# Performance work log

Measured on AMD Instinct MI355X. Metric: run time of the kernel, lower is better.

## Reference

```python
import jax, jax.numpy as jnp
import numpy as np

# Static module config (must match init_kwargs / input_specs)
C, HEADS, POINTS, LEVELS = 256, 8, 8, 2
H, W = 128, 128           # BEV grid per agent/level
NQ = H * W                # num_query = H*W
DH = C // HEADS           # per-head dim


def setup_inputs() -> dict:
    key = jax.random.key(0)
    ks = jax.random.split(key, 12)
    s = 0.02
    return {
        "query": jax.random.normal(ks[0], (1, NQ, C), jnp.float32),
        "query_pos": jax.random.normal(ks[1], (1, NQ, C), jnp.float32),
        "value": jax.random.normal(ks[2], (LEVELS, NQ, C), jnp.float32),
        "reference_points": jax.random.uniform(ks[3], (1, NQ, LEVELS, 2), jnp.float32),
        "spatial_shapes": jnp.full((LEVELS, 2), H, dtype=jnp.int32),
        "W_off": jax.random.normal(ks[4], (C, LEVELS * HEADS * POINTS * 2), jnp.float32) * s,
        "b_off": jax.random.normal(ks[5], (LEVELS * HEADS * POINTS * 2,), jnp.float32) * s,
        "W_attn": jax.random.normal(ks[6], (C, LEVELS * HEADS * POINTS), jnp.float32) * s,
        "b_attn": jax.random.normal(ks[7], (LEVELS * HEADS * POINTS,), jnp.float32) * s,
        "W_val": jax.random.normal(ks[8], (C, C), jnp.float32) * s,
        "b_val": jax.random.normal(ks[9], (C,), jnp.float32) * s,
        "W_out": jax.random.normal(ks[10], (C, C), jnp.float32) * s,
        "b_out": jax.random.normal(ks[11], (C,), jnp.float32) * s,
    }


def _bilinear(img, x, y):
    """grid_sample-style bilinear, align_corners=False, zero padding.
    img: (H, W, D); x, y: (...) pixel-space coords. Returns (..., D)."""
    Hh, Ww = img.shape[0], img.shape[1]
    x0f, y0f = jnp.floor(x), jnp.floor(y)
    x0, y0 = x0f.astype(jnp.int32), y0f.astype(jnp.int32)
    x1, y1 = x0 + 1, y0 + 1
    wx1, wy1 = x - x0f, y - y0f
    wx0, wy0 = 1.0 - wx1, 1.0 - wy1

    def gather(yy, xx):
        valid = (yy >= 0) & (yy < Hh) & (xx >= 0) & (xx < Ww)
        g = img[jnp.clip(yy, 0, Hh - 1), jnp.clip(xx, 0, Ww - 1)]
        return jnp.where(valid[..., None], g, 0.0)

    return (gather(y0, x0) * (wy0 * wx0)[..., None]
            + gather(y0, x1) * (wy0 * wx1)[..., None]
            + gather(y1, x0) * (wy1 * wx0)[..., None]
            + gather(y1, x1) * (wy1 * wx1)[..., None])


_sample_heads = jax.vmap(_bilinear, in_axes=(0, 0, 0))  # over heads


def reference(query, query_pos, value, reference_points, spatial_shapes,
              W_off, b_off, W_attn, b_attn, W_val, b_val, W_out, b_out):
    identity = query                                        # (1, NQ, C)
    q = (query + query_pos)[0]                              # (NQ, C), bs=1

    v = value @ W_val + b_val                               # (L, NQ, C)
    v = v.reshape(LEVELS, H, W, HEADS, DH)                  # per-level feature maps

    off = (q @ W_off + b_off).reshape(NQ, HEADS, LEVELS, POINTS, 2)
    attn = (q @ W_attn + b_attn).reshape(NQ, HEADS, LEVELS * POINTS)
    attn = jax.nn.softmax(attn, axis=-1).reshape(NQ, HEADS, LEVELS, POINTS)

    # offset_normalizer = (W, H) per level
    norm = jnp.stack([spatial_shapes[:, 1], spatial_shapes[:, 0]], -1).astype(q.dtype)  # (L, 2)
    # sampling_locations in normalized [0,1] coords: (NQ, HEADS, LEVELS, POINTS, 2)
    loc = reference_points[0][:, None, :, None, :] + off / norm[None, None, :, None, :]

    out = jnp.zeros((NQ, HEADS, DH), dtype=q.dtype)
    for l in range(LEVELS):
        img_l = jnp.transpose(v[l], (2, 0, 1, 3))           # (HEADS, H, W, DH)
        # align_corners=False: px = x_norm * W - 0.5
        xl = jnp.transpose(loc[:, :, l, :, 0], (1, 0, 2)) * W - 0.5  # (HEADS, NQ, POINTS)
        yl = jnp.transpose(loc[:, :, l, :, 1], (1, 0, 2)) * H - 0.5
        sampled = _sample_heads(img_l, xl, yl)              # (HEADS, NQ, POINTS, DH)
        out = out + jnp.einsum('hqpd,qhp->qhd', sampled, attn[:, :, l, :])

    out = out.reshape(NQ, C) @ W_out + b_out                # (NQ, C)
    return out[None] + identity                             # dropout is identity (eval / p=0)
```

## Files before the change

kernel.cpp:

```cpp
#include <hip/hip_runtime.h>
#include <hip/hip_bf16.h>
#include <math.h>

#define NQ     16384
#define CDIM   256
#define NHEADS 8
#define NPTS   8
#define NLVL   2
#define HH     128
#define WWID   128
#define DHEAD  32
#define NCAT   384

#define PW        130
#define CELLB     32
#define ROWB      (PW * CELLB)
#define MAPB      (PW * PW * CELLB)
#define BORDER_BLKS 16
#define TRANS_BLKS  224

typedef __bf16 bf16_t;
typedef __bf16 bf16x8 __attribute__((ext_vector_type(8)));
typedef float  f32x4  __attribute__((ext_vector_type(4)));
typedef float  f32x2  __attribute__((ext_vector_type(2)));

typedef __attribute__((address_space(1))) const uint32_t gau32;
typedef __attribute__((address_space(3))) uint32_t lau32;

__device__ __forceinline__ bf16_t f2b(float f) { return (bf16_t)f; }

__device__ __forceinline__ bf16x8 cvt8(float4 a, float4 b) {
    bf16x8 v;
    v[0] = f2b(a.x); v[1] = f2b(a.y); v[2] = f2b(a.z); v[3] = f2b(a.w);
    v[4] = f2b(b.x); v[5] = f2b(b.y); v[6] = f2b(b.z); v[7] = f2b(b.w);
    return v;
}

__global__ __launch_bounds__(256) void prep_k(const float* __restrict__ W_val,
                                              const float* __restrict__ W_off,
                                              const float* __restrict__ W_attn,
                                              const float* __restrict__ W_out,
                                              unsigned char* __restrict__ v2,
                                              bf16_t* __restrict__ Wt_val,
                                              bf16_t* __restrict__ Wt_qa,
                                              bf16_t* __restrict__ Wt_out) {
    const int b = blockIdx.x;
    if (b < BORDER_BLKS) {
        unsigned char* map = v2 + (size_t)b * MAPB;
        for (int i = threadIdx.x; i < 516; i += 256) {
            int y, x;
            if (i < 130)      { y = 0;        x = i;       }
            else if (i < 260) { y = 129;      x = i - 130; }
            else if (i < 388) { y = i - 259;  x = 0;       }
            else              { y = i - 387;  x = 129;     }
            uint4* p = reinterpret_cast<uint4*>(map + (size_t)y * ROWB + x * CELLB);
            p[0] = make_uint4(0, 0, 0, 0);
            p[1] = make_uint4(0, 0, 0, 0);
        }
        return;
    }
    {
        const int tb = b - BORDER_BLKS;
        const float* W; bf16_t* Wt; int N, t; bool permute = false;
        if (tb < 64)       { W = W_val;  Wt = Wt_val;            N = 256; t = tb;       permute = true; }
        else if (tb < 128) { W = W_off;  Wt = Wt_qa;             N = 256; t = tb - 64;  }
        else if (tb < 160) { W = W_attn; Wt = Wt_qa + 256 * 256; N = 128; t = tb - 128; }
        else               { W = W_out;  Wt = Wt_out;            N = 256; t = tb - 160; }
        const int ntn = N >> 5;
        const int k0 = (t / ntn) * 32, n0 = (t % ntn) * 32;
        const int tx = threadIdx.x & 31, ty = threadIdx.x >> 5;
        __shared__ float s[32][33];
#pragma unroll
        for (int i = 0; i < 4; ++i)
            s[ty + 8 * i][tx] = W[(size_t)(k0 + ty + 8 * i) * N + n0 + tx];
        __syncthreads();
#pragma unroll
        for (int i = 0; i < 4; ++i) {
            const int n = n0 + ty + 8 * i;
            const int p = permute ? ((n & ~63) | ((n & 3) << 4) | ((n & 63) >> 2)) : n;
            Wt[(size_t)p * 256 + k0 + tx] = f2b(s[tx][ty + 8 * i]);
        }
    }
}

template <int AMODE, bool PERM_V>
__device__ __forceinline__ void proj_body(bf16_t (&As)[2][64][64],
                                          int bidx, int bidy,
                                          const float* __restrict__ Af0,
                                          const float* __restrict__ Af1,
                                          const bf16_t* __restrict__ Bt,
                                          const float* __restrict__ bias,
                                          const float* __restrict__ bias2,
                                          int Nsplit,
                                          void* __restrict__ Cout,
                                          int N, int K) {
    const int tid  = threadIdx.x;
    const int wave = tid >> 6;
    const int lane = tid & 63;
    const int rowBase = bidy * 64;
    const int colBase = bidx * 128;
    const int wn = wave * 32;
    const int fr = lane & 15;
    const int fq = lane >> 4;

    f32x4 acc[4][2] = {};

    const int lrow = lane >> 3;
    const int scol = ((lane & 7) ^ lrow) * 8;

    auto loadA = [&](int t, float4 (&ra)[2][2]) {
#pragma unroll
        for (int tt = 0; tt < 2; ++tt) {
            const float* src =
                Af0 + (size_t)(rowBase + wave * 16 + tt * 8 + lrow) * K + t * 64 + scol;
            ra[tt][0] = *reinterpret_cast<const float4*>(src);
            ra[tt][1] = *reinterpret_cast<const float4*>(src + 4);
        }
    };
    auto loadA2 = [&](int t, float4 (&rb)[2][2]) {
#pragma unroll
        for (int tt = 0; tt < 2; ++tt) {
            const float* src =
                Af1 + (size_t)(rowBase + wave * 16 + tt * 8 + lrow) * K + t * 64 + scol;
            rb[tt][0] = *reinterpret_cast<const float4*>(src);
            rb[tt][1] = *reinterpret_cast<const float4*>(src + 4);
        }
    };
    auto storeA = [&](int buf, float4 (&ra)[2][2]) {
#pragma unroll
        for (int tt = 0; tt < 2; ++tt)
            *reinterpret_cast<bf16x8*>(
                &As[buf][wave * 16 + tt * 8 + lrow][(lane & 7) * 8]) =
                cvt8(ra[tt][0], ra[tt][1]);
    };
    auto storeAsum = [&](int buf, float4 (&ra)[2][2], float4 (&rb)[2][2]) {
#pragma unroll
        for (int tt = 0; tt < 2; ++tt) {
            float4 a = ra[tt][0], c = ra[tt][1];
            a.x += rb[tt][0].x; a.y += rb[tt][0].y;
            a.z += rb[tt][0].z; a.w += rb[tt][0].w;
            c.x += rb[tt][1].x; c.y += rb[tt][1].y;
            c.z += rb[tt][1].z; c.w += rb[tt][1].w;
            *reinterpret_cast<bf16x8*>(
                &As[buf][wave * 16 + tt * 8 + lrow][(lane & 7) * 8]) = cvt8(a, c);
        }
    };
    auto compute = [&](int c, int t) {
#pragma unroll
        for (int ks = 0; ks < 2; ++ks) {
            const int gk = ((ks * 4 + fq) ^ (fr & 7)) * 8;
            const int kb = t * 64 + (ks * 4 + fq) * 8;
            bf16x8 af[4], bfr[2];
#pragma unroll
            for (int i = 0; i < 4; ++i)
                af[i] = *reinterpret_cast<const bf16x8*>(&As[c][i * 16 + fr][gk]);
#pragma unroll
            for (int j = 0; j < 2; ++j)
                bfr[j] = *reinterpret_cast<const bf16x8*>(
                    &Bt[(size_t)(colBase + wn + j * 16 + fr) * K + kb]);
#pragma unroll
            for (int i = 0; i < 4; ++i)
#pragma unroll
                for (int j = 0; j < 2; ++j)
                    acc[i][j] = __builtin_amdgcn_mfma_f32_16x16x32_bf16(af[i], bfr[j],
                                                                        acc[i][j], 0, 0, 0);
        }
    };

    if constexpr (AMODE == 1) {
        float4 ra0[2][2], ra1[2][2];
        loadA(0, ra0);
        loadA(1, ra1);
        storeA(0, ra0);
        __syncthreads();
        loadA(2, ra0);
        compute(0, 0);
        storeA(1, ra1);
        __syncthreads();
        loadA(3, ra1);
        compute(1, 1);
        storeA(0, ra0);
        __syncthreads();
        compute(0, 2);
        storeA(1, ra1);
        __syncthreads();
        compute(1, 3);
    } else {
        float4 ra[2][2], rb[2][2];
        loadA(0, ra); loadA2(0, rb);
        storeAsum(0, ra, rb);
        __syncthreads();
        for (int t = 0; t < 4; ++t) {
            const int c = t & 1, n = c ^ 1;
            if (t + 1 < 4) { loadA(t + 1, ra); loadA2(t + 1, rb); }
            compute(c, t);
            if (t + 1 < 4) {
                storeAsum(n, ra, rb);
                __syncthreads();
            }
        }
    }

    if (PERM_V) {
        const int w2 = wave & 1;
        const int n0 = colBase + (wave >> 1) * 64 + fr * 4 + w2 * 2;
        const float bv0 = bias[n0], bv1 = bias[n0 + 1];
        const int hh = (n0 >> 5) & 7;
        const int dbase = n0 & 31;
        unsigned char* outp = (unsigned char*)Cout;
#pragma unroll
        for (int i = 0; i < 4; ++i) {
#pragma unroll
            for (int r = 0; r < 4; ++r) {
                const int row = rowBase + i * 16 + fq * 4 + r;
                const int lv = row >> 14, cell = row & 16383;
                const int y = cell >> 7, x = cell & 127;
                uint32_t pk = __builtin_amdgcn_cvt_pk_fp8_f32(
                    acc[i][0][r] + bv0, acc[i][1][r] + bv1, 0, false);
                *reinterpret_cast<unsigned short*>(
                    outp + (size_t)(lv * NHEADS + hh) * MAPB
                         + (size_t)(y + 1) * ROWB + (x + 1) * CELLB + dbase) =
                    (unsigned short)pk;
            }
        }
        return;
    }

#pragma unroll
    for (int j = 0; j < 2; ++j) {
        const int col = colBase + wn + j * 16 + fr;
        const float bv = (col < Nsplit) ? bias[col] : bias2[col - Nsplit];
#pragma unroll
        for (int i = 0; i < 4; ++i) {
#pragma unroll
            for (int r = 0; r < 4; ++r) {
                const int row = rowBase + i * 16 + fq * 4 + r;
                ((bf16_t*)Cout)[(size_t)row * N + col] = f2b(acc[i][j][r] + bv);
            }
        }
    }
}

__global__ __launch_bounds__(256, 4) void fused_proj_k(const float* __restrict__ value,
                                                       const float* __restrict__ query,
                                                       const float* __restrict__ query_pos,
                                                       const bf16_t* __restrict__ Wt_val,
                                                       const bf16_t* __restrict__ Wt_qa,
                                                       const float* __restrict__ b_val,
                                                       const float* __restrict__ b_off,
                                                       const float* __restrict__ b_attn,
                                                       unsigned char* __restrict__ v2,
                                                       bf16_t* __restrict__ cbuf) {
    __shared__ __align__(16) bf16_t As[2][64][64];
    const int b = blockIdx.x;
    if (b < 1024) {
        const int bidy = (b >> 4) * 8 + (b & 7);
        const int bidx = (b >> 3) & 1;
        proj_body<1, true>(As, bidx, bidy, value, nullptr,
                           Wt_val, b_val, b_val, 256, v2, CDIM, CDIM);
    } else {
        const int b2 = b - 1024;
        const int bidy = (b2 / 24) * 8 + (b2 & 7);
        const int bidx = (b2 >> 3) % 3;
        proj_body<2, false>(As, bidx, bidy, query, query_pos,
                            Wt_qa, b_off, b_attn, 256, cbuf, NCAT, CDIM);
    }
}

__global__ __launch_bounds__(256, 4) void outproj_k(const bf16_t* __restrict__ tmp,
                                                    const bf16_t* __restrict__ Wt_out,
                                                    const float* __restrict__ b_out,
                                                    const float* __restrict__ query,
                                                    float* __restrict__ out) {
    __shared__ __align__(16) bf16_t As[2][64][64];
    __shared__ __align__(16) bf16_t Bs[2][64][64];
    const int b = blockIdx.x;
    const int bidy = b >> 2, bidx = b & 3;
    const int tid = threadIdx.x, wave = tid >> 6, lane = tid & 63;
    const int rowBase = bidy * 64, colBase = bidx * 64;
    const int wm = (wave & 1) * 32, wn = (wave >> 1) * 32;
    const int fr = lane & 15, fq = lane >> 4;
    const int lrow = lane >> 3;
    const int K = 256;

    f32x4 acc[2][2] = {};

    auto stage = [&](int t, int buf) {
#pragma unroll
        for (int p = 0; p < 2; ++p) {
            const int row = wave * 16 + p * 8 + lrow;
            const int s = ((lane & 7) ^ (row & 7)) * 8;
            const bf16_t* srcA = tmp + (size_t)(rowBase + row) * K + t * 64 + s;
            __builtin_amdgcn_global_load_lds((gau32*)srcA,
                                             (lau32*)&As[buf][wave * 16 + p * 8][0],
                                             16, 0, 0);
            const bf16_t* srcB = Wt_out + (size_t)(colBase + row) * K + t * 64 + s;
            __builtin_amdgcn_global_load_lds((gau32*)srcB,
                                             (lau32*)&Bs[buf][wave * 16 + p * 8][0],
                                             16, 0, 0);
        }
    };

    stage(0, 0);
    __syncthreads();
    for (int t = 0; t < 4; ++t) {
        const int c = t & 1, n = c ^ 1;
        if (t + 1 < 4) stage(t + 1, n);
#pragma unroll
        for (int ks = 0; ks < 2; ++ks) {
            const int gk = ((ks * 4 + fq) ^ (fr & 7)) * 8;
            bf16x8 af[2], bfr[2];
#pragma unroll
            for (int i = 0; i < 2; ++i)
                af[i] = *reinterpret_cast<const bf16x8*>(&As[c][wm + i * 16 + fr][gk]);
#pragma unroll
            for (int j = 0; j < 2; ++j)
                bfr[j] = *reinterpret_cast<const bf16x8*>(&Bs[c][wn + j * 16 + fr][gk]);
#pragma unroll
            for (int i = 0; i < 2; ++i)
#pragma unroll
                for (int j = 0; j < 2; ++j)
                    acc[i][j] = __builtin_amdgcn_mfma_f32_16x16x32_bf16(af[i], bfr[j],
                                                                        acc[i][j], 0, 0, 0);
        }
        if (t + 1 < 4) __syncthreads();
    }

#pragma unroll
    for (int j = 0; j < 2; ++j) {
        const int col = colBase + wn + j * 16 + fr;
        const float bv = b_out[col];
#pragma unroll
        for (int i = 0; i < 2; ++i) {
#pragma unroll
            for (int r = 0; r < 4; ++r) {
                const int row = rowBase + wm + i * 16 + fq * 4 + r;
                out[(size_t)row * CDIM + col] =
                    acc[i][j][r] + bv + query[(size_t)row * CDIM + col];
            }
        }
    }
}

__device__ __forceinline__ void acc_tap2(uint2 u, float w, f32x2* acc2) {
    acc2[0] += __builtin_amdgcn_cvt_pk_f32_fp8((int)u.x, false) * w;
    acc2[1] += __builtin_amdgcn_cvt_pk_f32_fp8((int)u.x, true)  * w;
    acc2[2] += __builtin_amdgcn_cvt_pk_f32_fp8((int)u.y, false) * w;
    acc2[3] += __builtin_amdgcn_cvt_pk_f32_fp8((int)u.y, true)  * w;
}

__global__ __launch_bounds__(256, 8) void sample_k(const unsigned char* __restrict__ v2,
                                                   const bf16_t* __restrict__ cbuf,
                                                   const float* __restrict__ refp,
                                                   bf16_t* __restrict__ tmp) {
    const int b    = blockIdx.x;
    const int h    = b & 7;
    const int qblk = b >> 3;
    const int tid  = threadIdx.x;
    const int qloc = tid >> 2;
    const int ck   = tid & 3;
    const int q    = qblk * 64 + qloc;

    const bf16_t* qrow = cbuf + (size_t)q * NCAT;
    const float4 rp = *reinterpret_cast<const float4*>(refp + (size_t)q * 4);

    const bf16_t* attp = qrow + 256 + h * 16;
    bf16x8 A0 = *reinterpret_cast<const bf16x8*>(attp);
    bf16x8 A1 = *reinterpret_cast<const bf16x8*>(attp + 8);
    float e[16];
#pragma unroll
    for (int i = 0; i < 8; ++i) { e[i] = (float)A0[i]; e[8 + i] = (float)A1[i]; }
    float m = e[0];
#pragma unroll
    for (int i = 1; i < 16; ++i) m = fmaxf(m, e[i]);
    float s = 0.f;
#pragma unroll
    for (int i = 0; i < 16; ++i) { e[i] = __expf(e[i] - m); s += e[i]; }
    const float inv = 1.f / s;
#pragma unroll
    for (int i = 0; i < 16; ++i) e[i] *= inv;

    f32x2 acc2[4] = {};

#pragma unroll
    for (int l = 0; l < NLVL; ++l) {
        const float bx = (l == 0 ? rp.x : rp.z) * (float)WWID - 0.5f;
        const float by = (l == 0 ? rp.y : rp.w) * (float)HH - 0.5f;
        const unsigned char* base = v2 + (size_t)(l * NHEADS + h) * MAPB
                                       + 131 * CELLB + ck * 8;
        const bf16_t* offp = qrow + h * 32 + l * 16;
        bf16x8 o0 = *reinterpret_cast<const bf16x8*>(offp);
        bf16x8 o1 = *reinterpret_cast<const bf16x8*>(offp + 8);
        float ox[8], oy[8];
#pragma unroll
        for (int i = 0; i < 4; ++i) {
            ox[i]     = (float)o0[2 * i];  oy[i]     = (float)o0[2 * i + 1];
            ox[4 + i] = (float)o1[2 * i];  oy[4 + i] = (float)o1[2 * i + 1];
        }

#pragma unroll
        for (int p = 0; p < NPTS; ++p) {
            const float px = bx + ox[p];
            const float py = by + oy[p];
            const float w  = e[l * 8 + p];
            const float x0f = floorf(px), y0f = floorf(py);
            const int x0 = (int)x0f, y0 = (int)y0f;
            const float wx1 = px - x0f, wy1 = py - y0f;
            const float wx0 = 1.f - wx1, wy0 = 1.f - wy1;
            const int x0c = min(max(x0, -1), 128);
            const int x1c = min(max(x0 + 1, -1), 128);
            const int y0c = min(max(y0, -1), 128);
            const int y1c = min(max(y0 + 1, -1), 128);
            const unsigned char* r0 = base + y0c * ROWB;
            const unsigned char* r1 = base + y1c * ROWB;
            uint2 u00 = *reinterpret_cast<const uint2*>(r0 + x0c * CELLB);
            uint2 u10 = *reinterpret_cast<const uint2*>(r0 + x1c * CELLB);
            uint2 u01 = *reinterpret_cast<const uint2*>(r1 + x0c * CELLB);
            uint2 u11 = *reinterpret_cast<const uint2*>(r1 + x1c * CELLB);
            const float wy0w = w * wy0, wy1w = w * wy1;
            acc_tap2(u00, wy0w * wx0, acc2);
            acc_tap2(u10, wy0w * wx1, acc2);
            acc_tap2(u01, wy1w * wx0, acc2);
            acc_tap2(u11, wy1w * wx1, acc2);
        }
    }

    bf16x8 ov;
#pragma unroll
    for (int i = 0; i < 4; ++i) {
        ov[2 * i]     = f2b(acc2[i].x);
        ov[2 * i + 1] = f2b(acc2[i].y);
    }
    bf16_t* op = tmp + (size_t)q * CDIM + h * DHEAD + ck * 8;
    *reinterpret_cast<bf16x8*>(op) = ov;
}

extern "C" void kernel_launch(void* const* d_in, const int* in_sizes, int n_in,
                              void* d_out, int out_size, void* d_ws, size_t ws_size,
                              hipStream_t stream) {
    const float* query     = (const float*)d_in[0];
    const float* query_pos = (const float*)d_in[1];
    const float* value     = (const float*)d_in[2];
    const float* refp      = (const float*)d_in[3];
    const float* W_off  = (const float*)d_in[5];
    const float* b_off  = (const float*)d_in[6];
    const float* W_attn = (const float*)d_in[7];
    const float* b_attn = (const float*)d_in[8];
    const float* W_val  = (const float*)d_in[9];
    const float* b_val  = (const float*)d_in[10];
    const float* W_out  = (const float*)d_in[11];
    const float* b_out  = (const float*)d_in[12];
    float* out = (float*)d_out;

    char* ws = (char*)d_ws;
    unsigned char* v2 = (unsigned char*)(ws);
    bf16_t* cbuf    = (bf16_t*)(ws + 8654848);
    bf16_t* tmp     = (bf16_t*)(ws + 21237760);
    bf16_t* Wt_val  = (bf16_t*)(ws + 29626368);
    bf16_t* Wt_qa   = (bf16_t*)(ws + 29757440);
    bf16_t* Wt_out  = (bf16_t*)(ws + 29954048);

    prep_k<<<BORDER_BLKS + TRANS_BLKS, 256, 0, stream>>>(
        W_val, W_off, W_attn, W_out, v2, Wt_val, Wt_qa, Wt_out);
    fused_proj_k<<<1792, 256, 0, stream>>>(value, query, query_pos,
                                           Wt_val, Wt_qa, b_val, b_off, b_attn,
                                           v2, cbuf);
    sample_k<<<2048, 256, 0, stream>>>(v2, cbuf, refp, tmp);
    outproj_k<<<1024, 256, 0, stream>>>(tmp, Wt_out, b_out, query, out);
}
```

Measured before the change: 178.0 us.

## Fuse bilinear sampling with output projection through shared-memory tile

Merges the sampling kernel and the output-projection GEMM into one kernel. Each block now handles 16 queries across all 8 heads, with each thread covering 16 channels via 16-byte fp8 loads instead of 8. The sampled bf16 rows are written to a swizzled LDS tile, and MFMA then multiplies that tile by Wt_out read straight from global memory. This removes the intermediate tmp round-trip through HBM and one kernel launch. In exchange, Wt_out is reread by every block without LDS staging, and the 16-row GEMM tile is small, which may hurt MFMA efficiency and lower occupancy.

Result: slower. 190.5 us (+7.0%).

```diff
diff --git a/kernel.cpp b/kernel.cpp
--- a/kernel.cpp
+++ b/kernel.cpp
@@ -267,172 +267,152 @@
     }
 }
 
-__global__ __launch_bounds__(256, 4) void outproj_k(const bf16_t* __restrict__ tmp,
-                                                    const bf16_t* __restrict__ Wt_out,
-                                                    const float* __restrict__ b_out,
-                                                    const float* __restrict__ query,
-                                                    float* __restrict__ out) {
-    __shared__ __align__(16) bf16_t As[2][64][64];
-    __shared__ __align__(16) bf16_t Bs[2][64][64];
-    const int b = blockIdx.x;
-    const int bidy = b >> 2, bidx = b & 3;
-    const int tid = threadIdx.x, wave = tid >> 6, lane = tid & 63;
-    const int rowBase = bidy * 64, colBase = bidx * 64;
-    const int wm = (wave & 1) * 32, wn = (wave >> 1) * 32;
-    const int fr = lane & 15, fq = lane >> 4;
-    const int lrow = lane >> 3;
-    const int K = 256;
-
-    f32x4 acc[2][2] = {};
-
-    auto stage = [&](int t, int buf) {
-#pragma unroll
-        for (int p = 0; p < 2; ++p) {
-            const int row = wave * 16 + p * 8 + lrow;
-            const int s = ((lane & 7) ^ (row & 7)) * 8;
-            const bf16_t* srcA = tmp + (size_t)(rowBase + row) * K + t * 64 + s;
-            __builtin_amdgcn_global_load_lds((gau32*)srcA,
-                                             (lau32*)&As[buf][wave * 16 + p * 8][0],
-                                             16, 0, 0);
-            const bf16_t* srcB = Wt_out + (size_t)(colBase + row) * K + t * 64 + s;
-            __builtin_amdgcn_global_load_lds((gau32*)srcB,
-                                             (lau32*)&Bs[buf][wave * 16 + p * 8][0],
-                                             16, 0, 0);
-        }
-    };
-
-    stage(0, 0);
-    __syncthreads();
-    for (int t = 0; t < 4; ++t) {
-        const int c = t & 1, n = c ^ 1;
-        if (t + 1 < 4) stage(t + 1, n);
-#pragma unroll
-        for (int ks = 0; ks < 2; ++ks) {
-            const int gk = ((ks * 4 + fq) ^ (fr & 7)) * 8;
-            bf16x8 af[2], bfr[2];
-#pragma unroll
-            for (int i = 0; i < 2; ++i)
-                af[i] = *reinterpret_cast<const bf16x8*>(&As[c][wm + i * 16 + fr][gk]);
-#pragma unroll
-            for (int j = 0; j < 2; ++j)
-                bfr[j] = *reinterpret_cast<const bf16x8*>(&Bs[c][wn + j * 16 + fr][gk]);
-#pragma unroll
-            for (int i = 0; i < 2; ++i)
-#pragma unroll
-                for (int j = 0; j < 2; ++j)
-                    acc[i][j] = __builtin_amdgcn_mfma_f32_16x16x32_bf16(af[i], bfr[j],
-                                                                        acc[i][j], 0, 0, 0);
-        }
-        if (t + 1 < 4) __syncthreads();
-    }
-
-#pragma unroll
-    for (int j = 0; j < 2; ++j) {
-        const int col = colBase + wn + j * 16 + fr;
-        const float bv = b_out[col];
-#pragma unroll
-        for (int i = 0; i < 2; ++i) {
-#pragma unroll
-            for (int r = 0; r < 4; ++r) {
-                const int row = rowBase + wm + i * 16 + fq * 4 + r;
-                out[(size_t)row * CDIM + col] =
-                    acc[i][j][r] + bv + query[(size_t)row * CDIM + col];
-            }
-        }
-    }
-}
-
-__device__ __forceinline__ void acc_tap2(uint2 u, float w, f32x2* acc2) {
+__device__ __forceinline__ void acc_tap4(uint4 u, float w, f32x2* acc2) {
     acc2[0] += __builtin_amdgcn_cvt_pk_f32_fp8((int)u.x, false) * w;
     acc2[1] += __builtin_amdgcn_cvt_pk_f32_fp8((int)u.x, true)  * w;
     acc2[2] += __builtin_amdgcn_cvt_pk_f32_fp8((int)u.y, false) * w;
     acc2[3] += __builtin_amdgcn_cvt_pk_f32_fp8((int)u.y, true)  * w;
-}
-
-__global__ __launch_bounds__(256, 8) void sample_k(const unsigned char* __restrict__ v2,
-                                                   const bf16_t* __restrict__ cbuf,
-                                                   const float* __restrict__ refp,
-                                                   bf16_t* __restrict__ tmp) {
-    const int b    = blockIdx.x;
-    const int h    = b & 7;
-    const int qblk = b >> 3;
+    acc2[4] += __builtin_amdgcn_cvt_pk_f32_fp8((int)u.z, false) * w;
+    acc2[5] += __builtin_amdgcn_cvt_pk_f32_fp8((int)u.z, true)  * w;
+    acc2[6] += __builtin_amdgcn_cvt_pk_f32_fp8((int)u.w, false) * w;
+    acc2[7] += __builtin_amdgcn_cvt_pk_f32_fp8((int)u.w, true)  * w;
+}
+
+__global__ __launch_bounds__(256, 4) void sample_out_k(const unsigned char* __restrict__ v2,
+                                                       const bf16_t* __restrict__ cbuf,
+                                                       const float* __restrict__ refp,
+                                                       const bf16_t* __restrict__ Wt_out,
+                                                       const float* __restrict__ b_out,
+                                                       const float* __restrict__ query,
+                                                       float* __restrict__ out) {
+    __shared__ __align__(16) bf16_t Ls[16][256];
+    const int qblk = blockIdx.x;
     const int tid  = threadIdx.x;
-    const int qloc = tid >> 2;
-    const int ck   = tid & 3;
-    const int q    = qblk * 64 + qloc;
-
-    const bf16_t* qrow = cbuf + (size_t)q * NCAT;
-    const float4 rp = *reinterpret_cast<const float4*>(refp + (size_t)q * 4);
-
-    const bf16_t* attp = qrow + 256 + h * 16;
-    bf16x8 A0 = *reinterpret_cast<const bf16x8*>(attp);
-    bf16x8 A1 = *reinterpret_cast<const bf16x8*>(attp + 8);
-    float e[16];
-#pragma unroll
-    for (int i = 0; i < 8; ++i) { e[i] = (float)A0[i]; e[8 + i] = (float)A1[i]; }
-    float m = e[0];
-#pragma unroll
-    for (int i = 1; i < 16; ++i) m = fmaxf(m, e[i]);
-    float s = 0.f;
-#pragma unroll
-    for (int i = 0; i < 16; ++i) { e[i] = __expf(e[i] - m); s += e[i]; }
-    const float inv = 1.f / s;
-#pragma unroll
-    for (int i = 0; i < 16; ++i) e[i] *= inv;
-
-    f32x2 acc2[4] = {};
-
-#pragma unroll
-    for (int l = 0; l < NLVL; ++l) {
-        const float bx = (l == 0 ? rp.x : rp.z) * (float)WWID - 0.5f;
-        const float by = (l == 0 ? rp.y : rp.w) * (float)HH - 0.5f;
-        const unsigned char* base = v2 + (size_t)(l * NHEADS + h) * MAPB
-                                       + 131 * CELLB + ck * 8;
-        const bf16_t* offp = qrow + h * 32 + l * 16;
-        bf16x8 o0 = *reinterpret_cast<const bf16x8*>(offp);
-        bf16x8 o1 = *reinterpret_cast<const bf16x8*>(offp + 8);
-        float ox[8], oy[8];
+
+    {
+        const int ck   = tid & 1;
+        const int h    = (tid >> 1) & 7;
+        const int qloc = tid >> 4;
+        const int q    = qblk * 16 + qloc;
+
+        const bf16_t* qrow = cbuf + (size_t)q * NCAT;
+        const float4 rp = *reinterpret_cast<const float4*>(refp + (size_t)q * 4);
+
+        const bf16_t* attp = qrow + 256 + h * 16;
+        bf16x8 A0 = *reinterpret_cast<const bf16x8*>(attp);
+        bf16x8 A1 = *reinterpret_cast<const bf16x8*>(attp + 8);
+        float e[16];
+#pragma unroll
+        for (int i = 0; i < 8; ++i) { e[i] = (float)A0[i]; e[8 + i] = (float)A1[i]; }
+        float m = e[0];
+#pragma unroll
+        for (int i = 1; i < 16; ++i) m = fmaxf(m, e[i]);
+        float s = 0.f;
+#pragma unroll
+        for (int i = 0; i < 16; ++i) { e[i] = __expf(e[i] - m); s += e[i]; }
+        const float inv = 1.f / s;
+#pragma unroll
+        for (int i = 0; i < 16; ++i) e[i] *= inv;
+
+        f32x2 acc2[8] = {};
+
+#pragma unroll
+        for (int l = 0; l < NLVL; ++l) {
+            const float bx = (l == 0 ? rp.x : rp.z) * (float)WWID - 0.5f;
+            const float by = (l == 0 ? rp.y : rp.w) * (float)HH - 0.5f;
+            const unsigned char* base = v2 + (size_t)(l * NHEADS + h) * MAPB
+                                           + 131 * CELLB + ck * 16;
+            const bf16_t* offp = qrow + h * 32 + l * 16;
+            bf16x8 o0 = *reinterpret_cast<const bf16x8*>(offp);
+            bf16x8 o1 = *reinterpret_cast<const bf16x8*>(offp + 8);
+            float ox[8], oy[8];
+#pragma unroll
+            for (int i = 0; i < 4; ++i) {
+                ox[i]     = (float)o0[2 * i];  oy[i]     = (float)o0[2 * i + 1];
+                ox[4 + i] = (float)o1[2 * i];  oy[4 + i] = (float)o1[2 * i + 1];
+            }
+
+#pragma unroll
+            for (int p = 0; p < NPTS; ++p) {
+                const float px = bx + ox[p];
+                const float py = by + oy[p];
+                const float w  = e[l * 8 + p];
+                const float x0f = floorf(px), y0f = floorf(py);
+                const int x0 = (int)x0f, y0 = (int)y0f;
+                const float wx1 = px - x0f, wy1 = py - y0f;
+                const float wx0 = 1.f - wx1, wy0 = 1.f - wy1;
+                const int x0c = min(max(x0, -1), 128);
+                const int x1c = min(max(x0 + 1, -1), 128);
+                const int y0c = min(max(y0, -1), 128);
+                const int y1c = min(max(y0 + 1, -1), 128);
+                const unsigned char* r0 = base + y0c * ROWB;
+                const unsigned char* r1 = base + y1c * ROWB;
+                uint4 u00 = *reinterpret_cast<const uint4*>(r0 + x0c * CELLB);
+                uint4 u10 = *reinterpret_cast<const uint4*>(r0 + x1c * CELLB);
+                uint4 u01 = *reinterpret_cast<const uint4*>(r1 + x0c * CELLB);
+                uint4 u11 = *reinterpret_cast<const uint4*>(r1 + x1c * CELLB);
+                const float wy0w = w * wy0, wy1w = w * wy1;
+                acc_tap4(u00, wy0w * wx0, acc2);
+                acc_tap4(u10, wy0w * wx1, acc2);
+                acc_tap4(u01, wy1w * wx0, acc2);
+                acc_tap4(u11, wy1w * wx1, acc2);
+            }
+        }
+
+        bf16x8 ov0, ov1;
 #pragma unroll
         for (int i = 0; i < 4; ++i) {
-            ox[i]     = (float)o0[2 * i];  oy[i]     = (float)o0[2 * i + 1];
-            ox[4 + i] = (float)o1[2 * i];  oy[4 + i] = (float)o1[2 * i + 1];
-        }
-
-#pragma unroll
-        for (int p = 0; p < NPTS; ++p) {
-            const float px = bx + ox[p];
-            const float py = by + oy[p];
-            const float w  = e[l * 8 + p];
-            const float x0f = floorf(px), y0f = floorf(py);
-            const int x0 = (int)x0f, y0 = (int)y0f;
-            const float wx1 = px - x0f, wy1 = py - y0f;
-            const float wx0 = 1.f - wx1, wy0 = 1.f - wy1;
-            const int x0c = min(max(x0, -1), 128);
-            const int x1c = min(max(x0 + 1, -1), 128);
-            const int y0c = min(max(y0, -1), 128);
-            const int y1c = min(max(y0 + 1, -1), 128);
-            const unsigned char* r0 = base + y0c * ROWB;
-            const unsigned char* r1 = base + y1c * ROWB;
-            uint2 u00 = *reinterpret_cast<const uint2*>(r0 + x0c * CELLB);
-            uint2 u10 = *reinterpret_cast<const uint2*>(r0 + x1c * CELLB);
-            uint2 u01 = *reinterpret_cast<const uint2*>(r1 + x0c * CELLB);
-            uint2 u11 = *reinterpret_cast<const uint2*>(r1 + x1c * CELLB);
-            const float wy0w = w * wy0, wy1w = w * wy1;
-            acc_tap2(u00, wy0w * wx0, acc2);
-            acc_tap2(u10, wy0w * wx1, acc2);
-            acc_tap2(u01, wy1w * wx0, acc2);
-            acc_tap2(u11, wy1w * wx1, acc2);
-        }
-    }
-
-    bf16x8 ov;
-#pragma unroll
-    for (int i = 0; i < 4; ++i) {
-        ov[2 * i]     = f2b(acc2[i].x);
-        ov[2 * i + 1] = f2b(acc2[i].y);
-    }
-    bf16_t* op = tmp + (size_t)q * CDIM + h * DHEAD + ck * 8;
-    *reinterpret_cast<bf16x8*>(op) = ov;
+            ov0[2 * i]     = f2b(acc2[i].x);
+            ov0[2 * i + 1] = f2b(acc2[i].y);
+            ov1[2 * i]     = f2b(acc2[4 + i].x);
+            ov1[2 * i + 1] = f2b(acc2[4 + i].y);
+        }
+        const int c0 = h * 4 + ck * 2;
+        const int sw = qloc & 7;
+        *reinterpret_cast<bf16x8*>(&Ls[qloc][(c0 ^ sw) * 8])       = ov0;
+        *reinterpret_cast<bf16x8*>(&Ls[qloc][((c0 + 1) ^ sw) * 8]) = ov1;
+    }
+
+    __syncthreads();
+
+    {
+        const int wave = tid >> 6;
+        const int lane = tid & 63;
+        const int fr = lane & 15;
+        const int fq = lane >> 4;
+        const int colBase = wave * 64;
+        const int K = 256;
+
+        f32x4 acc[4] = {};
+#pragma unroll
+        for (int c32 = 0; c32 < 8; ++c32) {
+            const int gA = c32 * 4 + fq;
+            bf16x8 af = *reinterpret_cast<const bf16x8*>(
+                &Ls[fr][(gA ^ (fr & 7)) * 8]);
+            const int kb = c32 * 32 + fq * 8;
+            bf16x8 bfr[4];
+#pragma unroll
+            for (int j = 0; j < 4; ++j)
+                bfr[j] = *reinterpret_cast<const bf16x8*>(
+                    &Wt_out[(size_t)(colBase + j * 16 + fr) * K + kb]);
+#pragma unroll
+            for (int j = 0; j < 4; ++j)
+                acc[j] = __builtin_amdgcn_mfma_f32_16x16x32_bf16(af, bfr[j],
+                                                                 acc[j], 0, 0, 0);
+        }
+
+#pragma unroll
+        for (int j = 0; j < 4; ++j) {
+            const int col = colBase + j * 16 + fr;
+            const float bv = b_out[col];
+#pragma unroll
+            for (int r = 0; r < 4; ++r) {
+                const int row = qblk * 16 + fq * 4 + r;
+                out[(size_t)row * CDIM + col] =
+                    acc[j][r] + bv + query[(size_t)row * CDIM + col];
+            }
+        }
+    }
 }
 
 extern "C" void kernel_launch(void* const* d_in, const int* in_sizes, int n_in,
@@ -455,7 +435,6 @@
     char* ws = (char*)d_ws;
     unsigned char* v2 = (unsigned char*)(ws);
     bf16_t* cbuf    = (bf16_t*)(ws + 8654848);
-    bf16_t* tmp     = (bf16_t*)(ws + 21237760);
     bf16_t* Wt_val  = (bf16_t*)(ws + 29626368);
     bf16_t* Wt_qa   = (bf16_t*)(ws + 29757440);
     bf16_t* Wt_out  = (bf16_t*)(ws + 29954048);
@@ -465,6 +444,6 @@
     fused_proj_k<<<1792, 256, 0, stream>>>(value, query, query_pos,
                                            Wt_val, Wt_qa, b_val, b_off, b_attn,
                                            v2, cbuf);
-    sample_k<<<2048, 256, 0, stream>>>(v2, cbuf, refp, tmp);
-    outproj_k<<<1024, 256, 0, stream>>>(tmp, Wt_out, b_out, query, out);
-}
+    sample_out_k<<<1024, 256, 0, stream>>>(v2, cbuf, refp,
+                                           Wt_out, b_out, query, out);
+}
```
